# Performance work log

Hardware: AMD Instinct MI355X
Metric: run time of the kernel (lower is better)

The kernel has to match this reference:

```python
import jax, jax.numpy as jnp
import numpy as np

T = 128        # number of time points
D = 64         # flattened state dim (bs * z_dim, bs = 1)
H = 256        # hidden width of f-network
HK = 128       # hidden width of kernel network
MAX_IT = 3     # fixed-point iterations (args.max_iterations)


def setup_inputs() -> dict:
    key = jax.random.key(0)
    ks = jax.random.split(key, 6)
    g = lambda k, sh, sc: (jax.random.normal(k, sh, jnp.float32) * sc)
    z0 = jax.random.normal(ks[0], (1, D), jnp.float32)
    t = jnp.linspace(0.0, 1.0, T, dtype=jnp.float32)
    # f: D -> H -> D MLP (the 'func' integrand network)
    W1 = g(ks[1], (D, H), 1.0 / np.sqrt(D)); b1 = jnp.zeros((H,), jnp.float32)
    W2 = g(ks[2], (H, D), 1.0 / np.sqrt(H)); b2 = jnp.zeros((D,), jnp.float32)
    # kernel: (x, s) -> D*D matrix entries (the neural kernel K)
    Wk1 = g(ks[3], (2, HK), 1.0 / np.sqrt(2.0)); bk1 = jnp.zeros((HK,), jnp.float32)
    Wk2 = g(ks[4], (HK, D * D), 1.0 / np.sqrt(HK)); bk2 = jnp.zeros((D * D,), jnp.float32)
    return dict(z0=z0, t=t, W1=W1, b1=b1, W2=W2, b2=b2,
                Wk1=Wk1, bk1=bk1, Wk2=Wk2, bk2=bk2)


def _trapezoid_weights(t):
    """w[i, j]: trapezoid quadrature weight of node j for integral over [t0, t_i]."""
    dt = t[1] - t[0]  # uniform grid
    idx = jnp.arange(T)
    mask = (idx[None, :] <= idx[:, None]).astype(t.dtype)
    w = dt * mask
    w = w.at[(idx, idx)].multiply(0.5)   # halve right endpoint of each row
    w = w.at[:, 0].multiply(0.5)         # halve left endpoint
    w = w.at[0].set(0.0)                 # zero-length integral at t0
    return w


def _solve(z0, t, W1, b1, W2, b2, Wk1, bk1, Wk2, bk2):
    y0 = z0.reshape(-1)                                   # [D], solver flattens batch
    w = _trapezoid_weights(t)                             # [T, T]
    # Neural kernel K(x_i, s_j) -> [D, D], precomputed once on the grid.
    pairs = jnp.stack([jnp.broadcast_to(t[:, None], (T, T)),
                       jnp.broadcast_to(t[None, :], (T, T))], axis=-1)  # [T, T, 2]
    hK = jnp.tanh(pairs @ Wk1 + bk1)                      # [T, T, HK]
    K = (hK @ Wk2 + bk2).reshape(T, T, D, D)              # [T, T, D, D]

    def f(y):  # integrand network, applied over all time points
        return jnp.tanh(y @ W1 + b1) @ W2 + b2            # [T, D]

    def step(y, _):
        # G_i = \int_0^{x_i} K(x_i, s) f(y(s)) ds  (trapezoid on grid)
        G = jnp.einsum('ij,ijde,je->id', w, K, f(y))      # [T, D]
        # y'(x) = G(x)  =>  y_i = y0 + \int_0^{x_i} G(s) ds
        y_new = y0[None, :] + w @ G                       # [T, D]
        return y_new, None

    y_init = jnp.tile(y0[None, :], (T, 1))                # fixed-point initial guess
    y, _ = jax.lax.scan(step, y_init, None, length=MAX_IT)
    return y


def reference(z0, t, W1, b1, W2, b2, Wk1, bk1, Wk2, bk2):
    y = _solve(z0, t, W1, b1, W2, b2, Wk1, bk1, Wk2, bk2)  # [T, D]
    return y[-1].reshape(1, D)  # z[-1]: final state, shape [bs, dim]
```

## Files before the change

kernel.cpp:

```cpp
#include <hip/hip_runtime.h>
#include <hip/hip_bf16.h>

#define TT 128
#define DD 64
#define HH 256
#define HK 128
#define JH (TT*HK)
#define HD (HK*DD)
#define NCHUNK 64

__global__ void __launch_bounds__(256)
k_prep(const float* __restrict__ t, const float* __restrict__ Wk1,
       const float* __restrict__ bk1, const float* __restrict__ Wk2,
       float* __restrict__ A, float* __restrict__ Wk2t) {
    __shared__ float tile[32][65];
    int b = blockIdx.x, tid = threadIdx.x;
    if (b < 1024) {
        float dt = t[1] - t[0];
        #pragma unroll
        for (int k = 0; k < 8; ++k) {
            int idx = b * 2048 + k * 256 + tid;
            int h = idx & 127, j = (idx >> 7) & 127, i = idx >> 14;
            float w = (i == 0 || j > i) ? 0.f : dt * ((j == 0 || j == i) ? 0.5f : 1.0f);
            float v = tanhf(t[i] * Wk1[h] + t[j] * Wk1[HK + h] + bk1[h]);
            A[idx] = w * v;
        }
    } else {
        int bb = b - 1024;
        int h = bb >> 1, dh = (bb & 1) * 32;
        for (int k = tid; k < 32 * 64; k += 256) {
            int d = k >> 6, e = k & 63;
            tile[d][e] = Wk2[(size_t)h * (DD * DD) + (size_t)(dh + d) * DD + e];
        }
        __syncthreads();
        for (int k = tid; k < 64 * 32; k += 256) {
            int e = k >> 5, d = k & 31;
            Wk2t[(size_t)e * HD + h * DD + dh + d] = tile[d][e];
        }
    }
}

__global__ void __launch_bounds__(256)
k_f(const float* __restrict__ G, const float* __restrict__ z0,
    const float* __restrict__ t,
    const float* __restrict__ W1, const float* __restrict__ b1,
    const float* __restrict__ W2, const float* __restrict__ b2,
    const float* __restrict__ bk2,
    float* __restrict__ F, float* __restrict__ bF, int it) {
    int j = blockIdx.x, tid = threadIdx.x;
    int part = tid >> 6, d = tid & 63;
    __shared__ float red[4][64];
    __shared__ float ys[DD];
    __shared__ float hs[HH];
    __shared__ float fs[DD];
    float dt = t[1] - t[0];
    if (it == 0) {
        if (tid < DD) ys[tid] = z0[tid];
    } else {
        float s = 0.f;
        if (j > 0) {
            for (int jp = part; jp <= j; jp += 4) {
                float w = (jp == 0 || jp == j) ? 0.5f : 1.0f;
                s += w * G[jp * DD + d];
            }
        }
        red[part][d] = s;
        __syncthreads();
        if (part == 0)
            ys[d] = z0[d] + dt * (red[0][d] + red[1][d] + red[2][d] + red[3][d]);
    }
    __syncthreads();
    float acc = b1[tid];
    #pragma unroll 8
    for (int e = 0; e < DD; ++e) acc += ys[e] * W1[e * HH + tid];
    hs[tid] = tanhf(acc);
    __syncthreads();
    {
        float s = 0.f;
        #pragma unroll 8
        for (int h = part * 64; h < part * 64 + 64; ++h) s += hs[h] * W2[h * DD + d];
        red[part][d] = s;
    }
    __syncthreads();
    if (part == 0) {
        float a = b2[d] + red[0][d] + red[1][d] + red[2][d] + red[3][d];
        fs[d] = a;
        F[j * DD + d] = a;
    }
    __syncthreads();
    {
        float s = 0.f;
        #pragma unroll
        for (int e = part * 16; e < part * 16 + 16; ++e) s += bk2[d * DD + e] * fs[e];
        red[part][d] = s;
    }
    __syncthreads();
    if (part == 0)
        bF[j * DD + d] = red[0][d] + red[1][d] + red[2][d] + red[3][d];
}

__global__ void __launch_bounds__(256)
k_M(const float* __restrict__ F, const float* __restrict__ Wk2t,
    float* __restrict__ M) {
    int tid = threadIdx.x;
    int hd = blockIdx.x * 256 + tid;
    int j0 = blockIdx.y * 8;
    __shared__ __attribute__((aligned(16))) float Fs[8][64];
    for (int k = tid; k < 8 * DD; k += 256) Fs[k >> 6][k & 63] = F[j0 * DD + k];
    __syncthreads();
    float acc[8];
    #pragma unroll
    for (int k = 0; k < 8; ++k) acc[k] = 0.f;
    const float* Wp = Wk2t + hd;
    for (int e = 0; e < DD; e += 8) {
        float w0 = Wp[(size_t)(e+0) * HD];
        float w1 = Wp[(size_t)(e+1) * HD];
        float w2 = Wp[(size_t)(e+2) * HD];
        float w3 = Wp[(size_t)(e+3) * HD];
        float w4 = Wp[(size_t)(e+4) * HD];
        float w5 = Wp[(size_t)(e+5) * HD];
        float w6 = Wp[(size_t)(e+6) * HD];
        float w7 = Wp[(size_t)(e+7) * HD];
        #pragma unroll
        for (int k = 0; k < 8; ++k) {
            float4 f0 = *(const float4*)&Fs[k][e];
            float4 f1 = *(const float4*)&Fs[k][e + 4];
            acc[k] += f0.x*w0 + f0.y*w1 + f0.z*w2 + f0.w*w3
                    + f1.x*w4 + f1.y*w5 + f1.z*w6 + f1.w*w7;
        }
    }
    #pragma unroll
    for (int k = 0; k < 8; ++k) M[(size_t)(j0 + k) * HD + hd] = acc[k];
}

__global__ void __launch_bounds__(256)
k_G1(const float* __restrict__ A, const float* __restrict__ M,
     float* __restrict__ P) {
    int itile = blockIdx.x, c = blockIdx.y;
    if (c > 4 * itile + 3) return;
    __shared__ __attribute__((aligned(16))) float As[8 * 256];
    __shared__ float red[4][8][64];
    int tid = threadIdx.x, sub = tid >> 6, d = tid & 63;
    {
        const float* Ab = A + (size_t)itile * 8 * JH + c * 256;
        float4* As4 = (float4*)As;
        #pragma unroll
        for (int k = 0; k < 2; ++k) {
            int idx = tid + k * 256;
            int r = idx >> 6, q = idx & 63;
            As4[idx] = *(const float4*)(Ab + (size_t)r * JH + q * 4);
        }
    }
    __syncthreads();
    float acc[8] = {0.f,0.f,0.f,0.f,0.f,0.f,0.f,0.f};
    const float* Mp = M + ((size_t)c * 256) * DD + d;
    int jl0 = sub * 64;
    for (int jl = jl0; jl < jl0 + 64; jl += 8) {
        float m0 = Mp[(size_t)(jl + 0) * DD];
        float m1 = Mp[(size_t)(jl + 1) * DD];
        float m2 = Mp[(size_t)(jl + 2) * DD];
        float m3 = Mp[(size_t)(jl + 3) * DD];
        float m4 = Mp[(size_t)(jl + 4) * DD];
        float m5 = Mp[(size_t)(jl + 5) * DD];
        float m6 = Mp[(size_t)(jl + 6) * DD];
        float m7 = Mp[(size_t)(jl + 7) * DD];
        #pragma unroll
        for (int r = 0; r < 8; ++r) {
            float4 a0 = *(const float4*)&As[r * 256 + jl];
            float4 a1 = *(const float4*)&As[r * 256 + jl + 4];
            acc[r] += a0.x*m0 + a0.y*m1 + a0.z*m2 + a0.w*m3
                    + a1.x*m4 + a1.y*m5 + a1.z*m6 + a1.w*m7;
        }
    }
    #pragma unroll
    for (int r = 0; r < 8; ++r) red[sub][r][d] = acc[r];
    __syncthreads();
    if (sub == 0) {
        #pragma unroll
        for (int r = 0; r < 8; ++r) {
            float v = red[0][r][d] + red[1][r][d] + red[2][r][d] + red[3][r][d];
            P[(size_t)c * (TT * DD) + (itile * 8 + r) * DD + d] = v;
        }
    }
}

__global__ void __launch_bounds__(256)
k_Gfin(const float* __restrict__ P, const float* __restrict__ bF,
       const float* __restrict__ t, float* __restrict__ G) {
    int j = blockIdx.x, tid = threadIdx.x;
    int part = tid >> 6, d = tid & 63;
    __shared__ float red[4][64];
    float dt = t[1] - t[0];
    float a = 0.f;
    int cmax = j >> 1;
    for (int c = part; c <= cmax; c += 4) a += P[(size_t)c * (TT * DD) + j * DD + d];
    if (j > 0) {
        float s = 0.f;
        for (int jp = part; jp <= j; jp += 4) {
            float w = (jp == 0 || jp == j) ? 0.5f : 1.0f;
            s += w * bF[jp * DD + d];
        }
        a += dt * s;
    }
    red[part][d] = a;
    __syncthreads();
    if (part == 0)
        G[j * DD + d] = red[0][d] + red[1][d] + red[2][d] + red[3][d];
}

__global__ void __launch_bounds__(256)
k_out(const float* __restrict__ G, const float* __restrict__ z0,
      const float* __restrict__ t, float* __restrict__ out) {
    int tid = threadIdx.x, part = tid >> 6, d = tid & 63;
    __shared__ float red[4][64];
    float dt = t[1] - t[0];
    float s = 0.f;
    for (int j = part; j < TT; j += 4) {
        float w = (j == 0 || j == TT - 1) ? 0.5f : 1.0f;
        s += w * G[j * DD + d];
    }
    red[part][d] = s;
    __syncthreads();
    if (part == 0)
        out[d] = z0[d] + dt * (red[0][d] + red[1][d] + red[2][d] + red[3][d]);
}

extern "C" void kernel_launch(void* const* d_in, const int* in_sizes, int n_in,
                              void* d_out, int out_size, void* d_ws, size_t ws_size,
                              hipStream_t stream) {
    const float* z0  = (const float*)d_in[0];
    const float* t   = (const float*)d_in[1];
    const float* W1  = (const float*)d_in[2];
    const float* b1  = (const float*)d_in[3];
    const float* W2  = (const float*)d_in[4];
    const float* b2  = (const float*)d_in[5];
    const float* Wk1 = (const float*)d_in[6];
    const float* bk1 = (const float*)d_in[7];
    const float* Wk2 = (const float*)d_in[8];
    const float* bk2 = (const float*)d_in[9];
    float* out = (float*)d_out;

    float* ws   = (float*)d_ws;
    float* A    = ws;
    float* Wk2t = A    + (size_t)TT*TT*HK;
    float* M    = Wk2t + (size_t)HK*DD*DD;
    float* F    = M    + (size_t)TT*HK*DD;
    float* bF   = F    + TT*DD;
    float* G    = bF   + TT*DD;
    float* P    = G    + TT*DD;

    k_prep<<<1280, 256, 0, stream>>>(t, Wk1, bk1, Wk2, A, Wk2t);

    for (int it = 0; it < 3; ++it) {
        k_f<<<TT, 256, 0, stream>>>(G, z0, t, W1, b1, W2, b2, bk2, F, bF, it);
        k_M<<<dim3(32, 16), 256, 0, stream>>>(F, Wk2t, M);
        k_G1<<<dim3(16, NCHUNK), 256, 0, stream>>>(A, M, P);
        k_Gfin<<<TT, 256, 0, stream>>>(P, bF, t, G);
    }
    k_out<<<1, 256, 0, stream>>>(G, z0, t, out);
}
```

Baseline: 208.4 us.

## Fuse partial-sum reduction into G1 via atomics and fold first f-pass into prep

Removes the k_Gfin kernel by having k_G1 atomically accumulate its chunk partials directly into a double-buffered G array, with chunk 0 adding the bF trapezoid term. The first iteration's MLP evaluation is folded into extra blocks of k_prep, and k_F zeroes the next G buffer while reading the previous one. This cuts kernel launches and the P scratch round-trip per iteration. In exchange it adds atomic contention and makes the float summation order nondeterministic.

After: 256.3 us. 23.0% more time.

```diff
diff --git a/kernel.cpp b/kernel.cpp
--- a/kernel.cpp
+++ b/kernel.cpp
@@ -9,11 +9,58 @@
 #define HD (HK*DD)
 #define NCHUNK 64
 
+__device__ __forceinline__ void mlp_from_ys(
+    const float* __restrict__ ys, float* __restrict__ hs, float* __restrict__ fs,
+    float (*red)[64],
+    const float* __restrict__ W1, const float* __restrict__ b1,
+    const float* __restrict__ W2, const float* __restrict__ b2,
+    const float* __restrict__ bk2,
+    float* __restrict__ F, float* __restrict__ bF, int j, int tid)
+{
+    int part = tid >> 6, d = tid & 63;
+    float acc = b1[tid];
+    #pragma unroll 8
+    for (int e = 0; e < DD; ++e) acc += ys[e] * W1[e * HH + tid];
+    hs[tid] = tanhf(acc);
+    __syncthreads();
+    {
+        float s = 0.f;
+        #pragma unroll 8
+        for (int h = part * 64; h < part * 64 + 64; ++h) s += hs[h] * W2[h * DD + d];
+        red[part][d] = s;
+    }
+    __syncthreads();
+    if (part == 0) {
+        float a = b2[d] + red[0][d] + red[1][d] + red[2][d] + red[3][d];
+        fs[d] = a;
+        F[j * DD + d] = a;
+    }
+    __syncthreads();
+    {
+        float s = 0.f;
+        #pragma unroll
+        for (int e = part * 16; e < part * 16 + 16; ++e) s += bk2[d * DD + e] * fs[e];
+        red[part][d] = s;
+    }
+    __syncthreads();
+    if (part == 0)
+        bF[j * DD + d] = red[0][d] + red[1][d] + red[2][d] + red[3][d];
+}
+
 __global__ void __launch_bounds__(256)
 k_prep(const float* __restrict__ t, const float* __restrict__ Wk1,
        const float* __restrict__ bk1, const float* __restrict__ Wk2,
-       float* __restrict__ A, float* __restrict__ Wk2t) {
+       const float* __restrict__ z0,
+       const float* __restrict__ W1, const float* __restrict__ b1,
+       const float* __restrict__ W2, const float* __restrict__ b2,
+       const float* __restrict__ bk2,
+       float* __restrict__ A, float* __restrict__ Wk2t,
+       float* __restrict__ F, float* __restrict__ bF, float* __restrict__ G0) {
     __shared__ float tile[32][65];
+    __shared__ float red[4][64];
+    __shared__ float ys[DD];
+    __shared__ float hs[HH];
+    __shared__ float fs[DD];
     int b = blockIdx.x, tid = threadIdx.x;
     if (b < 1024) {
         float dt = t[1] - t[0];
@@ -25,7 +72,7 @@
             float v = tanhf(t[i] * Wk1[h] + t[j] * Wk1[HK + h] + bk1[h]);
             A[idx] = w * v;
         }
-    } else {
+    } else if (b < 1280) {
         int bb = b - 1024;
         int h = bb >> 1, dh = (bb & 1) * 32;
         for (int k = tid; k < 32 * 64; k += 256) {
@@ -37,16 +84,21 @@
             int e = k >> 5, d = k & 31;
             Wk2t[(size_t)e * HD + h * DD + dh + d] = tile[d][e];
         }
-    }
-}
-
-__global__ void __launch_bounds__(256)
-k_f(const float* __restrict__ G, const float* __restrict__ z0,
-    const float* __restrict__ t,
+    } else {
+        int j = b - 1280;
+        if (tid < DD) { ys[tid] = z0[tid]; G0[j * DD + tid] = 0.f; }
+        __syncthreads();
+        mlp_from_ys(ys, hs, fs, red, W1, b1, W2, b2, bk2, F, bF, j, tid);
+    }
+}
+
+__global__ void __launch_bounds__(256)
+k_F(const float* __restrict__ Gr, float* __restrict__ Gz,
+    const float* __restrict__ z0, const float* __restrict__ t,
     const float* __restrict__ W1, const float* __restrict__ b1,
     const float* __restrict__ W2, const float* __restrict__ b2,
     const float* __restrict__ bk2,
-    float* __restrict__ F, float* __restrict__ bF, int it) {
+    float* __restrict__ F, float* __restrict__ bF) {
     int j = blockIdx.x, tid = threadIdx.x;
     int part = tid >> 6, d = tid & 63;
     __shared__ float red[4][64];
@@ -54,49 +106,20 @@
     __shared__ float hs[HH];
     __shared__ float fs[DD];
     float dt = t[1] - t[0];
-    if (it == 0) {
-        if (tid < DD) ys[tid] = z0[tid];
-    } else {
-        float s = 0.f;
-        if (j > 0) {
-            for (int jp = part; jp <= j; jp += 4) {
-                float w = (jp == 0 || jp == j) ? 0.5f : 1.0f;
-                s += w * G[jp * DD + d];
-            }
-        }
-        red[part][d] = s;
-        __syncthreads();
-        if (part == 0)
-            ys[d] = z0[d] + dt * (red[0][d] + red[1][d] + red[2][d] + red[3][d]);
-    }
-    __syncthreads();
-    float acc = b1[tid];
-    #pragma unroll 8
-    for (int e = 0; e < DD; ++e) acc += ys[e] * W1[e * HH + tid];
-    hs[tid] = tanhf(acc);
-    __syncthreads();
-    {
-        float s = 0.f;
-        #pragma unroll 8
-        for (int h = part * 64; h < part * 64 + 64; ++h) s += hs[h] * W2[h * DD + d];
-        red[part][d] = s;
-    }
-    __syncthreads();
-    if (part == 0) {
-        float a = b2[d] + red[0][d] + red[1][d] + red[2][d] + red[3][d];
-        fs[d] = a;
-        F[j * DD + d] = a;
-    }
-    __syncthreads();
-    {
-        float s = 0.f;
-        #pragma unroll
-        for (int e = part * 16; e < part * 16 + 16; ++e) s += bk2[d * DD + e] * fs[e];
-        red[part][d] = s;
-    }
+    if (tid < DD) Gz[j * DD + tid] = 0.f;
+    float s = 0.f;
+    if (j > 0) {
+        for (int jp = part; jp <= j; jp += 4) {
+            float w = (jp == 0 || jp == j) ? 0.5f : 1.0f;
+            s += w * Gr[jp * DD + d];
+        }
+    }
+    red[part][d] = s;
     __syncthreads();
     if (part == 0)
-        bF[j * DD + d] = red[0][d] + red[1][d] + red[2][d] + red[3][d];
+        ys[d] = z0[d] + dt * (red[0][d] + red[1][d] + red[2][d] + red[3][d]);
+    __syncthreads();
+    mlp_from_ys(ys, hs, fs, red, W1, b1, W2, b2, bk2, F, bF, j, tid);
 }
 
 __global__ void __launch_bounds__(256)
@@ -135,7 +158,8 @@
 
 __global__ void __launch_bounds__(256)
 k_G1(const float* __restrict__ A, const float* __restrict__ M,
-     float* __restrict__ P) {
+     const float* __restrict__ bF, const float* __restrict__ t,
+     float* __restrict__ Gout) {
     int itile = blockIdx.x, c = blockIdx.y;
     if (c > 4 * itile + 3) return;
     __shared__ __attribute__((aligned(16))) float As[8 * 256];
@@ -179,33 +203,26 @@
         #pragma unroll
         for (int r = 0; r < 8; ++r) {
             float v = red[0][r][d] + red[1][r][d] + red[2][r][d] + red[3][r][d];
-            P[(size_t)c * (TT * DD) + (itile * 8 + r) * DD + d] = v;
-        }
-    }
-}
-
-__global__ void __launch_bounds__(256)
-k_Gfin(const float* __restrict__ P, const float* __restrict__ bF,
-       const float* __restrict__ t, float* __restrict__ G) {
-    int j = blockIdx.x, tid = threadIdx.x;
-    int part = tid >> 6, d = tid & 63;
-    __shared__ float red[4][64];
-    float dt = t[1] - t[0];
-    float a = 0.f;
-    int cmax = j >> 1;
-    for (int c = part; c <= cmax; c += 4) a += P[(size_t)c * (TT * DD) + j * DD + d];
-    if (j > 0) {
-        float s = 0.f;
-        for (int jp = part; jp <= j; jp += 4) {
-            float w = (jp == 0 || jp == j) ? 0.5f : 1.0f;
-            s += w * bF[jp * DD + d];
-        }
-        a += dt * s;
-    }
-    red[part][d] = a;
-    __syncthreads();
-    if (part == 0)
-        G[j * DD + d] = red[0][d] + red[1][d] + red[2][d] + red[3][d];
+            atomicAdd(&Gout[(itile * 8 + r) * DD + d], v);
+        }
+        if (c == 0) {
+            float dt = t[1] - t[0];
+            int jbase = itile * 8;
+            float b0 = 0.5f * bF[d];
+            float rs = 0.f;
+            for (int p = 1; p < jbase; ++p) rs += bF[p * DD + d];
+            #pragma unroll
+            for (int r = 0; r < 8; ++r) {
+                int j = jbase + r;
+                float bj = bF[j * DD + d];
+                if (j > 0) {
+                    float val = dt * (b0 + rs + 0.5f * bj);
+                    atomicAdd(&Gout[j * DD + d], val);
+                    rs += bj;
+                }
+            }
+        }
+    }
 }
 
 __global__ void __launch_bounds__(256)
@@ -246,16 +263,21 @@
     float* M    = Wk2t + (size_t)HK*DD*DD;
     float* F    = M    + (size_t)TT*HK*DD;
     float* bF   = F    + TT*DD;
-    float* G    = bF   + TT*DD;
-    float* P    = G    + TT*DD;
-
-    k_prep<<<1280, 256, 0, stream>>>(t, Wk1, bk1, Wk2, A, Wk2t);
-
+    float* Gb0  = bF   + TT*DD;
+    float* Gb1  = Gb0  + TT*DD;
+
+    k_prep<<<1408, 256, 0, stream>>>(t, Wk1, bk1, Wk2, z0,
+                                     W1, b1, W2, b2, bk2, A, Wk2t, F, bF, Gb0);
+
+    float* Gbuf[2] = { Gb0, Gb1 };
     for (int it = 0; it < 3; ++it) {
-        k_f<<<TT, 256, 0, stream>>>(G, z0, t, W1, b1, W2, b2, bk2, F, bF, it);
+        float* Gacc = Gbuf[it & 1];
+        if (it > 0) {
+            float* Gprev = Gbuf[(it + 1) & 1];
+            k_F<<<TT, 256, 0, stream>>>(Gprev, Gacc, z0, t, W1, b1, W2, b2, bk2, F, bF);
+        }
         k_M<<<dim3(32, 16), 256, 0, stream>>>(F, Wk2t, M);
-        k_G1<<<dim3(16, NCHUNK), 256, 0, stream>>>(A, M, P);
-        k_Gfin<<<TT, 256, 0, stream>>>(P, bF, t, G);
-    }
-    k_out<<<1, 256, 0, stream>>>(G, z0, t, out);
-}
+        k_G1<<<dim3(16, NCHUNK), 256, 0, stream>>>(A, M, bF, t, Gacc);
+    }
+    k_out<<<1, 256, 0, stream>>>(Gb0, z0, t, out);
+}
```

## Fuse f-network into M kernel and merge G partial-sum kernels per row

Applied to the files above, without the earlier changes.

Merges the f-MLP into the M-projection kernel, so each block recomputes f for its 8 time points instead of reading F from a separate launch. It also replaces the chunked k_G1 partial-product kernel and the k_Gfin reduction with one kernel that handles one output row i. That cuts each iteration from four launches to two and drops the P and F buffers. In exchange, the MLP is computed redundantly across 32 column blocks. The row-per-block G kernel also loses the shared-memory A tile reuse across 8 rows, has heavily imbalanced work across rows and launches only 128 blocks.

Result: slower. 629.8 us (+202.2%).

```diff
diff --git a/kernel.cpp b/kernel.cpp
--- a/kernel.cpp
+++ b/kernel.cpp
@@ -7,7 +7,6 @@
 #define HK 128
 #define JH (TT*HK)
 #define HD (HK*DD)
-#define NCHUNK 64
 
 __global__ void __launch_bounds__(256)
 k_prep(const float* __restrict__ t, const float* __restrict__ Wk1,
@@ -41,76 +40,104 @@
 }
 
 __global__ void __launch_bounds__(256)
-k_f(const float* __restrict__ G, const float* __restrict__ z0,
-    const float* __restrict__ t,
-    const float* __restrict__ W1, const float* __restrict__ b1,
-    const float* __restrict__ W2, const float* __restrict__ b2,
-    const float* __restrict__ bk2,
-    float* __restrict__ F, float* __restrict__ bF, int it) {
-    int j = blockIdx.x, tid = threadIdx.x;
-    int part = tid >> 6, d = tid & 63;
-    __shared__ float red[4][64];
-    __shared__ float ys[DD];
-    __shared__ float hs[HH];
-    __shared__ float fs[DD];
+k_FM(const float* __restrict__ G, const float* __restrict__ z0,
+     const float* __restrict__ t,
+     const float* __restrict__ W1, const float* __restrict__ b1,
+     const float* __restrict__ W2, const float* __restrict__ b2,
+     const float* __restrict__ bk2, const float* __restrict__ Wk2t,
+     float* __restrict__ M, float* __restrict__ bF, int it) {
+    int bx = blockIdx.x;
+    int j0 = blockIdx.y * 8;
+    int tid = threadIdx.x, part = tid >> 6, d = tid & 63;
+    __shared__ float ys[8][DD];
+    __shared__ float hs[8][HH];
+    __shared__ float red[4][8][DD];
+    __shared__ __attribute__((aligned(16))) float Fs[8][DD];
     float dt = t[1] - t[0];
+
     if (it == 0) {
-        if (tid < DD) ys[tid] = z0[tid];
+        if (tid < DD) {
+            float z = z0[tid];
+            #pragma unroll
+            for (int r = 0; r < 8; ++r) ys[r][tid] = z;
+        }
     } else {
         float s = 0.f;
-        if (j > 0) {
-            for (int jp = part; jp <= j; jp += 4) {
-                float w = (jp == 0 || jp == j) ? 0.5f : 1.0f;
-                s += w * G[jp * DD + d];
+        for (int jp = 1 + part; jp < j0; jp += 4) s += G[jp * DD + d];
+        red[part][0][d] = s;
+        __syncthreads();
+        if (part == 0) {
+            float g0 = G[d];
+            float run = red[0][0][d] + red[1][0][d] + red[2][0][d] + red[3][0][d];
+            float base = z0[d];
+            #pragma unroll
+            for (int r = 0; r < 8; ++r) {
+                int j = j0 + r;
+                float gj = G[j * DD + d];
+                ys[r][d] = (j == 0) ? base
+                                    : base + dt * (0.5f * g0 + run + 0.5f * gj);
+                if (j > 0) run += gj;
             }
         }
-        red[part][d] = s;
+    }
+    __syncthreads();
+
+    float acc[8];
+    {
+        float bb = b1[tid];
+        #pragma unroll
+        for (int r = 0; r < 8; ++r) acc[r] = bb;
+    }
+    for (int e = 0; e < DD; ++e) {
+        float w1v = W1[e * HH + tid];
+        #pragma unroll
+        for (int r = 0; r < 8; ++r) acc[r] += ys[r][e] * w1v;
+    }
+    #pragma unroll
+    for (int r = 0; r < 8; ++r) hs[r][tid] = tanhf(acc[r]);
+    __syncthreads();
+
+    {
+        float a2[8] = {0.f,0.f,0.f,0.f,0.f,0.f,0.f,0.f};
+        for (int h = part * 64; h < part * 64 + 64; ++h) {
+            float w2v = W2[h * DD + d];
+            #pragma unroll
+            for (int r = 0; r < 8; ++r) a2[r] += hs[r][h] * w2v;
+        }
+        #pragma unroll
+        for (int r = 0; r < 8; ++r) red[part][r][d] = a2[r];
+    }
+    __syncthreads();
+    {
+        #pragma unroll
+        for (int rr = 0; rr < 2; ++rr) {
+            int r = part * 2 + rr;
+            Fs[r][d] = b2[d] + red[0][r][d] + red[1][r][d] +
+                       red[2][r][d] + red[3][r][d];
+        }
+    }
+    __syncthreads();
+
+    if (bx == 0) {
+        float a3[8] = {0.f,0.f,0.f,0.f,0.f,0.f,0.f,0.f};
+        for (int e = part * 16; e < part * 16 + 16; ++e) {
+            float bv = bk2[d * DD + e];
+            #pragma unroll
+            for (int r = 0; r < 8; ++r) a3[r] += Fs[r][e] * bv;
+        }
+        #pragma unroll
+        for (int r = 0; r < 8; ++r) red[part][r][d] = a3[r];
         __syncthreads();
-        if (part == 0)
-            ys[d] = z0[d] + dt * (red[0][d] + red[1][d] + red[2][d] + red[3][d]);
-    }
-    __syncthreads();
-    float acc = b1[tid];
-    #pragma unroll 8
-    for (int e = 0; e < DD; ++e) acc += ys[e] * W1[e * HH + tid];
-    hs[tid] = tanhf(acc);
-    __syncthreads();
-    {
-        float s = 0.f;
-        #pragma unroll 8
-        for (int h = part * 64; h < part * 64 + 64; ++h) s += hs[h] * W2[h * DD + d];
-        red[part][d] = s;
-    }
-    __syncthreads();
-    if (part == 0) {
-        float a = b2[d] + red[0][d] + red[1][d] + red[2][d] + red[3][d];
-        fs[d] = a;
-        F[j * DD + d] = a;
-    }
-    __syncthreads();
-    {
-        float s = 0.f;
-        #pragma unroll
-        for (int e = part * 16; e < part * 16 + 16; ++e) s += bk2[d * DD + e] * fs[e];
-        red[part][d] = s;
-    }
-    __syncthreads();
-    if (part == 0)
-        bF[j * DD + d] = red[0][d] + red[1][d] + red[2][d] + red[3][d];
-}
-
-__global__ void __launch_bounds__(256)
-k_M(const float* __restrict__ F, const float* __restrict__ Wk2t,
-    float* __restrict__ M) {
-    int tid = threadIdx.x;
-    int hd = blockIdx.x * 256 + tid;
-    int j0 = blockIdx.y * 8;
-    __shared__ __attribute__((aligned(16))) float Fs[8][64];
-    for (int k = tid; k < 8 * DD; k += 256) Fs[k >> 6][k & 63] = F[j0 * DD + k];
-    __syncthreads();
-    float acc[8];
-    #pragma unroll
-    for (int k = 0; k < 8; ++k) acc[k] = 0.f;
+        #pragma unroll
+        for (int rr = 0; rr < 2; ++rr) {
+            int r = part * 2 + rr;
+            bF[(j0 + r) * DD + d] = red[0][r][d] + red[1][r][d] +
+                                    red[2][r][d] + red[3][r][d];
+        }
+    }
+
+    int hd = bx * 256 + tid;
+    float macc[8] = {0.f,0.f,0.f,0.f,0.f,0.f,0.f,0.f};
     const float* Wp = Wk2t + hd;
     for (int e = 0; e < DD; e += 8) {
         float w0 = Wp[(size_t)(e+0) * HD];
@@ -122,90 +149,57 @@
         float w6 = Wp[(size_t)(e+6) * HD];
         float w7 = Wp[(size_t)(e+7) * HD];
         #pragma unroll
-        for (int k = 0; k < 8; ++k) {
-            float4 f0 = *(const float4*)&Fs[k][e];
-            float4 f1 = *(const float4*)&Fs[k][e + 4];
-            acc[k] += f0.x*w0 + f0.y*w1 + f0.z*w2 + f0.w*w3
-                    + f1.x*w4 + f1.y*w5 + f1.z*w6 + f1.w*w7;
+        for (int r = 0; r < 8; ++r) {
+            float4 f0 = *(const float4*)&Fs[r][e];
+            float4 f1 = *(const float4*)&Fs[r][e + 4];
+            macc[r] += f0.x*w0 + f0.y*w1 + f0.z*w2 + f0.w*w3
+                     + f1.x*w4 + f1.y*w5 + f1.z*w6 + f1.w*w7;
         }
     }
     #pragma unroll
-    for (int k = 0; k < 8; ++k) M[(size_t)(j0 + k) * HD + hd] = acc[k];
-}
-
-__global__ void __launch_bounds__(256)
-k_G1(const float* __restrict__ A, const float* __restrict__ M,
-     float* __restrict__ P) {
-    int itile = blockIdx.x, c = blockIdx.y;
-    if (c > 4 * itile + 3) return;
-    __shared__ __attribute__((aligned(16))) float As[8 * 256];
-    __shared__ float red[4][8][64];
-    int tid = threadIdx.x, sub = tid >> 6, d = tid & 63;
-    {
-        const float* Ab = A + (size_t)itile * 8 * JH + c * 256;
-        float4* As4 = (float4*)As;
-        #pragma unroll
-        for (int k = 0; k < 2; ++k) {
-            int idx = tid + k * 256;
-            int r = idx >> 6, q = idx & 63;
-            As4[idx] = *(const float4*)(Ab + (size_t)r * JH + q * 4);
-        }
-    }
-    __syncthreads();
-    float acc[8] = {0.f,0.f,0.f,0.f,0.f,0.f,0.f,0.f};
-    const float* Mp = M + ((size_t)c * 256) * DD + d;
-    int jl0 = sub * 64;
-    for (int jl = jl0; jl < jl0 + 64; jl += 8) {
-        float m0 = Mp[(size_t)(jl + 0) * DD];
-        float m1 = Mp[(size_t)(jl + 1) * DD];
-        float m2 = Mp[(size_t)(jl + 2) * DD];
-        float m3 = Mp[(size_t)(jl + 3) * DD];
-        float m4 = Mp[(size_t)(jl + 4) * DD];
-        float m5 = Mp[(size_t)(jl + 5) * DD];
-        float m6 = Mp[(size_t)(jl + 6) * DD];
-        float m7 = Mp[(size_t)(jl + 7) * DD];
-        #pragma unroll
-        for (int r = 0; r < 8; ++r) {
-            float4 a0 = *(const float4*)&As[r * 256 + jl];
-            float4 a1 = *(const float4*)&As[r * 256 + jl + 4];
-            acc[r] += a0.x*m0 + a0.y*m1 + a0.z*m2 + a0.w*m3
-                    + a1.x*m4 + a1.y*m5 + a1.z*m6 + a1.w*m7;
-        }
-    }
-    #pragma unroll
-    for (int r = 0; r < 8; ++r) red[sub][r][d] = acc[r];
-    __syncthreads();
-    if (sub == 0) {
-        #pragma unroll
-        for (int r = 0; r < 8; ++r) {
-            float v = red[0][r][d] + red[1][r][d] + red[2][r][d] + red[3][r][d];
-            P[(size_t)c * (TT * DD) + (itile * 8 + r) * DD + d] = v;
-        }
-    }
-}
-
-__global__ void __launch_bounds__(256)
-k_Gfin(const float* __restrict__ P, const float* __restrict__ bF,
-       const float* __restrict__ t, float* __restrict__ G) {
-    int j = blockIdx.x, tid = threadIdx.x;
-    int part = tid >> 6, d = tid & 63;
+    for (int r = 0; r < 8; ++r) M[(size_t)(j0 + r) * HD + hd] = macc[r];
+}
+
+__global__ void __launch_bounds__(256)
+k_G(const float* __restrict__ A, const float* __restrict__ M,
+    const float* __restrict__ bF, const float* __restrict__ t,
+    float* __restrict__ G) {
+    int i = blockIdx.x, tid = threadIdx.x;
+    int sub = tid >> 6, d = tid & 63;
     __shared__ float red[4][64];
     float dt = t[1] - t[0];
-    float a = 0.f;
-    int cmax = j >> 1;
-    for (int c = part; c <= cmax; c += 4) a += P[(size_t)c * (TT * DD) + j * DD + d];
-    if (j > 0) {
+
+    int Q = (i + 1) * (HK / 4);
+    const float* Arow = A + (size_t)i * JH;
+    float acc = 0.f;
+    int jh0 = sub * Q;
+    for (int jj = jh0; jj < jh0 + Q; jj += 8) {
+        float4 a0 = *(const float4*)(Arow + jj);
+        float4 a1 = *(const float4*)(Arow + jj + 4);
+        const float* Mb = M + (size_t)jj * DD + d;
+        float m0 = Mb[0 * DD];
+        float m1 = Mb[1 * DD];
+        float m2 = Mb[2 * DD];
+        float m3 = Mb[3 * DD];
+        float m4 = Mb[4 * DD];
+        float m5 = Mb[5 * DD];
+        float m6 = Mb[6 * DD];
+        float m7 = Mb[7 * DD];
+        acc += a0.x*m0 + a0.y*m1 + a0.z*m2 + a0.w*m3
+             + a1.x*m4 + a1.y*m5 + a1.z*m6 + a1.w*m7;
+    }
+    if (i > 0) {
         float s = 0.f;
-        for (int jp = part; jp <= j; jp += 4) {
-            float w = (jp == 0 || jp == j) ? 0.5f : 1.0f;
+        for (int jp = sub; jp <= i; jp += 4) {
+            float w = (jp == 0 || jp == i) ? 0.5f : 1.0f;
             s += w * bF[jp * DD + d];
         }
-        a += dt * s;
-    }
-    red[part][d] = a;
-    __syncthreads();
-    if (part == 0)
-        G[j * DD + d] = red[0][d] + red[1][d] + red[2][d] + red[3][d];
+        acc += dt * s;
+    }
+    red[sub][d] = acc;
+    __syncthreads();
+    if (sub == 0)
+        G[i * DD + d] = red[0][d] + red[1][d] + red[2][d] + red[3][d];
 }
 
 __global__ void __launch_bounds__(256)
@@ -244,18 +238,15 @@
     float* A    = ws;
     float* Wk2t = A    + (size_t)TT*TT*HK;
     float* M    = Wk2t + (size_t)HK*DD*DD;
-    float* F    = M    + (size_t)TT*HK*DD;
-    float* bF   = F    + TT*DD;
+    float* bF   = M    + (size_t)TT*HK*DD;
     float* G    = bF   + TT*DD;
-    float* P    = G    + TT*DD;
 
     k_prep<<<1280, 256, 0, stream>>>(t, Wk1, bk1, Wk2, A, Wk2t);
 
     for (int it = 0; it < 3; ++it) {
-        k_f<<<TT, 256, 0, stream>>>(G, z0, t, W1, b1, W2, b2, bk2, F, bF, it);
-        k_M<<<dim3(32, 16), 256, 0, stream>>>(F, Wk2t, M);
-        k_G1<<<dim3(16, NCHUNK), 256, 0, stream>>>(A, M, P);
-        k_Gfin<<<TT, 256, 0, stream>>>(P, bF, t, G);
+        k_FM<<<dim3(32, 16), 256, 0, stream>>>(G, z0, t, W1, b1, W2, b2,
+                                               bk2, Wk2t, M, bF, it);
+        k_G<<<TT, 256, 0, stream>>>(A, M, bF, t, G);
     }
     k_out<<<1, 256, 0, stream>>>(G, z0, t, out);
 }
```

## Remove prep kernel: compute kernel-net activations on the fly and read Wk2 directly

Applied to the files above, without the earlier changes.

Drops the precompute kernel that materialized the weighted tanh activation tensor A (T*T*HK floats) and a transposed copy of Wk2. k_G1 now recomputes the weighted tanh values into shared memory, and k_M reads Wk2 rows directly with float4 loads instead of strided reads from the transposed copy. The final output kernel is folded into the last iteration's k_Gfin through atomicAdd, with out initialized to z0 inside k_G1. This removes one large write/read pass and two launches, at the cost of redundant tanh evaluation in every iteration. The atomic output relies on ordering: k_G1 must finish writing z0 before k_Gfin adds, which stream order guarantees.

Result: faster. 201.5 us (-3.3%).

```diff
diff --git a/kernel.cpp b/kernel.cpp
--- a/kernel.cpp
+++ b/kernel.cpp
@@ -10,38 +10,7 @@
 #define NCHUNK 64
 
 __global__ void __launch_bounds__(256)
-k_prep(const float* __restrict__ t, const float* __restrict__ Wk1,
-       const float* __restrict__ bk1, const float* __restrict__ Wk2,
-       float* __restrict__ A, float* __restrict__ Wk2t) {
-    __shared__ float tile[32][65];
-    int b = blockIdx.x, tid = threadIdx.x;
-    if (b < 1024) {
-        float dt = t[1] - t[0];
-        #pragma unroll
-        for (int k = 0; k < 8; ++k) {
-            int idx = b * 2048 + k * 256 + tid;
-            int h = idx & 127, j = (idx >> 7) & 127, i = idx >> 14;
-            float w = (i == 0 || j > i) ? 0.f : dt * ((j == 0 || j == i) ? 0.5f : 1.0f);
-            float v = tanhf(t[i] * Wk1[h] + t[j] * Wk1[HK + h] + bk1[h]);
-            A[idx] = w * v;
-        }
-    } else {
-        int bb = b - 1024;
-        int h = bb >> 1, dh = (bb & 1) * 32;
-        for (int k = tid; k < 32 * 64; k += 256) {
-            int d = k >> 6, e = k & 63;
-            tile[d][e] = Wk2[(size_t)h * (DD * DD) + (size_t)(dh + d) * DD + e];
-        }
-        __syncthreads();
-        for (int k = tid; k < 64 * 32; k += 256) {
-            int e = k >> 5, d = k & 31;
-            Wk2t[(size_t)e * HD + h * DD + dh + d] = tile[d][e];
-        }
-    }
-}
-
-__global__ void __launch_bounds__(256)
-k_f(const float* __restrict__ G, const float* __restrict__ z0,
+k_F(const float* __restrict__ G, const float* __restrict__ z0,
     const float* __restrict__ t,
     const float* __restrict__ W1, const float* __restrict__ b1,
     const float* __restrict__ W2, const float* __restrict__ b2,
@@ -100,7 +69,7 @@
 }
 
 __global__ void __launch_bounds__(256)
-k_M(const float* __restrict__ F, const float* __restrict__ Wk2t,
+k_M(const float* __restrict__ F, const float* __restrict__ Wk2,
     float* __restrict__ M) {
     int tid = threadIdx.x;
     int hd = blockIdx.x * 256 + tid;
@@ -108,50 +77,50 @@
     __shared__ __attribute__((aligned(16))) float Fs[8][64];
     for (int k = tid; k < 8 * DD; k += 256) Fs[k >> 6][k & 63] = F[j0 * DD + k];
     __syncthreads();
-    float acc[8];
+    float acc[8] = {0.f,0.f,0.f,0.f,0.f,0.f,0.f,0.f};
+    const float* Wrow = Wk2 + (size_t)(hd >> 6) * (DD * DD) + (size_t)(hd & 63) * DD;
+    for (int e = 0; e < DD; e += 8) {
+        float4 wa = *(const float4*)(Wrow + e);
+        float4 wb = *(const float4*)(Wrow + e + 4);
+        #pragma unroll
+        for (int r = 0; r < 8; ++r) {
+            float4 f0 = *(const float4*)&Fs[r][e];
+            float4 f1 = *(const float4*)&Fs[r][e + 4];
+            acc[r] += f0.x*wa.x + f0.y*wa.y + f0.z*wa.z + f0.w*wa.w
+                    + f1.x*wb.x + f1.y*wb.y + f1.z*wb.z + f1.w*wb.w;
+        }
+    }
     #pragma unroll
-    for (int k = 0; k < 8; ++k) acc[k] = 0.f;
-    const float* Wp = Wk2t + hd;
-    for (int e = 0; e < DD; e += 8) {
-        float w0 = Wp[(size_t)(e+0) * HD];
-        float w1 = Wp[(size_t)(e+1) * HD];
-        float w2 = Wp[(size_t)(e+2) * HD];
-        float w3 = Wp[(size_t)(e+3) * HD];
-        float w4 = Wp[(size_t)(e+4) * HD];
-        float w5 = Wp[(size_t)(e+5) * HD];
-        float w6 = Wp[(size_t)(e+6) * HD];
-        float w7 = Wp[(size_t)(e+7) * HD];
-        #pragma unroll
-        for (int k = 0; k < 8; ++k) {
-            float4 f0 = *(const float4*)&Fs[k][e];
-            float4 f1 = *(const float4*)&Fs[k][e + 4];
-            acc[k] += f0.x*w0 + f0.y*w1 + f0.z*w2 + f0.w*w3
-                    + f1.x*w4 + f1.y*w5 + f1.z*w6 + f1.w*w7;
-        }
-    }
-    #pragma unroll
-    for (int k = 0; k < 8; ++k) M[(size_t)(j0 + k) * HD + hd] = acc[k];
-}
-
-__global__ void __launch_bounds__(256)
-k_G1(const float* __restrict__ A, const float* __restrict__ M,
-     float* __restrict__ P) {
+    for (int r = 0; r < 8; ++r) M[(size_t)(j0 + r) * HD + hd] = acc[r];
+}
+
+__global__ void __launch_bounds__(256)
+k_G1(const float* __restrict__ t, const float* __restrict__ Wk1,
+     const float* __restrict__ bk1, const float* __restrict__ M,
+     float* __restrict__ P, const float* __restrict__ z0,
+     float* __restrict__ out, int final_it) {
     int itile = blockIdx.x, c = blockIdx.y;
     if (c > 4 * itile + 3) return;
     __shared__ __attribute__((aligned(16))) float As[8 * 256];
     __shared__ float red[4][8][64];
     int tid = threadIdx.x, sub = tid >> 6, d = tid & 63;
+
     {
-        const float* Ab = A + (size_t)itile * 8 * JH + c * 256;
-        float4* As4 = (float4*)As;
-        #pragma unroll
-        for (int k = 0; k < 2; ++k) {
-            int idx = tid + k * 256;
-            int r = idx >> 6, q = idx & 63;
-            As4[idx] = *(const float4*)(Ab + (size_t)r * JH + q * 4);
-        }
-    }
-    __syncthreads();
+        float dt = t[1] - t[0];
+        int h = tid & 127;
+        int j = 2 * c + (tid >> 7);
+        float wk0 = Wk1[h], wk1v = Wk1[HK + h], bk = bk1[h];
+        float tj = t[j];
+        #pragma unroll
+        for (int k = 0; k < 8; ++k) {
+            int i = itile * 8 + k;
+            float w = (i == 0 || j > i) ? 0.f : dt * ((j == 0 || j == i) ? 0.5f : 1.0f);
+            As[k * 256 + tid] = w * tanhf(t[i] * wk0 + tj * wk1v + bk);
+        }
+    }
+    if (final_it && itile == 0 && c == 0 && tid < DD) out[tid] = z0[tid];
+    __syncthreads();
+
     float acc[8] = {0.f,0.f,0.f,0.f,0.f,0.f,0.f,0.f};
     const float* Mp = M + ((size_t)c * 256) * DD + d;
     int jl0 = sub * 64;
@@ -186,7 +155,8 @@
 
 __global__ void __launch_bounds__(256)
 k_Gfin(const float* __restrict__ P, const float* __restrict__ bF,
-       const float* __restrict__ t, float* __restrict__ G) {
+       const float* __restrict__ t, float* __restrict__ G,
+       float* __restrict__ out, int final_it) {
     int j = blockIdx.x, tid = threadIdx.x;
     int part = tid >> 6, d = tid & 63;
     __shared__ float red[4][64];
@@ -204,25 +174,14 @@
     }
     red[part][d] = a;
     __syncthreads();
-    if (part == 0)
-        G[j * DD + d] = red[0][d] + red[1][d] + red[2][d] + red[3][d];
-}
-
-__global__ void __launch_bounds__(256)
-k_out(const float* __restrict__ G, const float* __restrict__ z0,
-      const float* __restrict__ t, float* __restrict__ out) {
-    int tid = threadIdx.x, part = tid >> 6, d = tid & 63;
-    __shared__ float red[4][64];
-    float dt = t[1] - t[0];
-    float s = 0.f;
-    for (int j = part; j < TT; j += 4) {
-        float w = (j == 0 || j == TT - 1) ? 0.5f : 1.0f;
-        s += w * G[j * DD + d];
-    }
-    red[part][d] = s;
-    __syncthreads();
-    if (part == 0)
-        out[d] = z0[d] + dt * (red[0][d] + red[1][d] + red[2][d] + red[3][d]);
+    if (part == 0) {
+        float v = red[0][d] + red[1][d] + red[2][d] + red[3][d];
+        G[j * DD + d] = v;
+        if (final_it) {
+            float wj = (j == 0 || j == TT - 1) ? 0.5f : 1.0f;
+            atomicAdd(&out[d], dt * wj * v);
+        }
+    }
 }
 
 extern "C" void kernel_launch(void* const* d_in, const int* in_sizes, int n_in,
@@ -240,22 +199,18 @@
     const float* bk2 = (const float*)d_in[9];
     float* out = (float*)d_out;
 
-    float* ws   = (float*)d_ws;
-    float* A    = ws;
-    float* Wk2t = A    + (size_t)TT*TT*HK;
-    float* M    = Wk2t + (size_t)HK*DD*DD;
-    float* F    = M    + (size_t)TT*HK*DD;
-    float* bF   = F    + TT*DD;
-    float* G    = bF   + TT*DD;
-    float* P    = G    + TT*DD;
-
-    k_prep<<<1280, 256, 0, stream>>>(t, Wk1, bk1, Wk2, A, Wk2t);
+    float* ws = (float*)d_ws;
+    float* M  = ws;
+    float* F  = M  + (size_t)TT*HK*DD;
+    float* bF = F  + TT*DD;
+    float* G  = bF + TT*DD;
+    float* P  = G  + TT*DD;
 
     for (int it = 0; it < 3; ++it) {
-        k_f<<<TT, 256, 0, stream>>>(G, z0, t, W1, b1, W2, b2, bk2, F, bF, it);
-        k_M<<<dim3(32, 16), 256, 0, stream>>>(F, Wk2t, M);
-        k_G1<<<dim3(16, NCHUNK), 256, 0, stream>>>(A, M, P);
-        k_Gfin<<<TT, 256, 0, stream>>>(P, bF, t, G);
-    }
-    k_out<<<1, 256, 0, stream>>>(G, z0, t, out);
-}
+        int fin = (it == 2) ? 1 : 0;
+        k_F<<<TT, 256, 0, stream>>>(G, z0, t, W1, b1, W2, b2, bk2, F, bF, it);
+        k_M<<<dim3(32, 16), 256, 0, stream>>>(F, Wk2, M);
+        k_G1<<<dim3(16, NCHUNK), 256, 0, stream>>>(t, Wk1, bk1, M, P, z0, out, fin);
+        k_Gfin<<<TT, 256, 0, stream>>>(P, bF, t, G, out, fin);
+    }
+}
```
